# Kernel optimization log

Hardware: AMD Instinct MI355X
Metric: run time of the kernel (lower is better)

## Reference

```python
import jax, jax.numpy as jnp
import numpy as np

D_MODEL = 512
D_STATE = 16
D_CONV = 2
DT_RANK = D_MODEL // 16  # mamba default dt_rank = ceil(d_model/16)
D_INNER = D_MODEL        # expand = 1
B, L = 4, 2048
LN_EPS = 1e-5


def setup_inputs() -> dict:
    key = jax.random.key(0)
    ks = jax.random.split(key, 16)
    s = 0.02
    inp = {
        "x_signal": jax.random.normal(ks[0], (B, L, D_MODEL), jnp.float32),
        "x_stats": jax.random.normal(ks[1], (B, 1, D_MODEL), jnp.float32),
        # GatedCrossAttention params (torch Linear weight layout: (out, in))
        "gW1": jax.random.normal(ks[2], (D_MODEL, 2 * D_MODEL), jnp.float32) * s,
        "gb1": jnp.zeros((D_MODEL,), jnp.float32),
        "gW2": jax.random.normal(ks[3], (1, D_MODEL), jnp.float32) * s,
        "gb2": jnp.zeros((1,), jnp.float32),
        "ln_g": jnp.ones((D_MODEL,), jnp.float32),
        "ln_b": jnp.zeros((D_MODEL,), jnp.float32),
        # Mamba params
        "in_proj_W": jax.random.normal(ks[4], (2 * D_INNER, D_MODEL), jnp.float32) * s,
        "conv_w": jax.random.normal(ks[5], (D_INNER, D_CONV), jnp.float32) * s,
        "conv_b": jnp.zeros((D_INNER,), jnp.float32),
        "x_proj_W": jax.random.normal(ks[6], (DT_RANK + 2 * D_STATE, D_INNER), jnp.float32) * s,
        "dt_proj_W": jax.random.normal(ks[7], (D_INNER, DT_RANK), jnp.float32) * s,
        "dt_proj_b": jnp.full((D_INNER,), -4.6, jnp.float32),  # softplus ~ 0.01
        "A_log": jnp.log(jnp.broadcast_to(jnp.arange(1, D_STATE + 1, dtype=jnp.float32), (D_INNER, D_STATE))),
        "Dp": jnp.ones((D_INNER,), jnp.float32),
        "out_proj_W": jax.random.normal(ks[8], (D_MODEL, D_INNER), jnp.float32) * s,
    }
    return inp


def _silu(x):
    return x * jax.nn.sigmoid(x)


def _forward(x_signal, x_stats, gW1, gb1, gW2, gb2, ln_g, ln_b,
             in_proj_W, conv_w, conv_b, x_proj_W, dt_proj_W, dt_proj_b,
             A_log, Dp, out_proj_W):
    # ---- GatedCrossAttention ----
    xs = jnp.broadcast_to(x_stats, x_signal.shape)           # (B,L,D)
    gi = jnp.concatenate([x_signal, xs], axis=-1)            # (B,L,2D)
    h = jax.nn.relu(gi @ gW1.T + gb1)
    gate = jax.nn.sigmoid(h @ gW2.T + gb2)                   # (B,L,1)
    x = x_signal + gate * xs
    mu = jnp.mean(x, -1, keepdims=True)
    var = jnp.var(x, -1, keepdims=True)
    x = (x - mu) * jax.lax.rsqrt(var + LN_EPS) * ln_g + ln_b  # (B,L,D)

    # ---- Mamba (d_state=16, d_conv=2, expand=1) ----
    xz = x @ in_proj_W.T                                     # (B,L,2*Din)
    u, z = jnp.split(xz, 2, axis=-1)
    # causal depthwise conv1d, kernel size 2
    up = jnp.pad(u, ((0, 0), (D_CONV - 1, 0), (0, 0)))
    uc = conv_b + sum(conv_w[:, k] * up[:, k:k + u.shape[1]] for k in range(D_CONV))
    u = _silu(uc)                                            # (B,L,Din)

    xdbc = u @ x_proj_W.T                                    # (B,L,dt_rank+2N)
    dt = xdbc[..., :DT_RANK]
    Bm = xdbc[..., DT_RANK:DT_RANK + D_STATE]                # (B,L,N)
    Cm = xdbc[..., DT_RANK + D_STATE:]                       # (B,L,N)
    delta = jax.nn.softplus(dt @ dt_proj_W.T + dt_proj_b)    # (B,L,Din)

    A = -jnp.exp(A_log)                                      # (Din,N)
    dA = jnp.exp(delta[..., None] * A)                       # (B,L,Din,N)
    dBu = delta[..., None] * Bm[:, :, None, :] * u[..., None]

    def step(hst, inps):
        dA_t, dBu_t, C_t = inps
        hst = dA_t * hst + dBu_t                             # (B,Din,N)
        y_t = jnp.einsum('bdn,bn->bd', hst, C_t)
        return hst, y_t

    h0 = jnp.zeros((u.shape[0], D_INNER, D_STATE), u.dtype)
    xs_scan = (jnp.swapaxes(dA, 0, 1), jnp.swapaxes(dBu, 0, 1), jnp.swapaxes(Cm, 0, 1))
    _, ys = jax.lax.scan(step, h0, xs_scan)                  # (L,B,Din)
    y = jnp.swapaxes(ys, 0, 1) + Dp * u
    y = y * _silu(z)
    out = y @ out_proj_W.T                                   # (B,L,D)
    # dropout is identity in eval mode
    return out


def reference(x_signal, x_stats, gW1, gb1, gW2, gb2, ln_g, ln_b,
              in_proj_W, conv_w, conv_b, x_proj_W, dt_proj_W, dt_proj_b,
              A_log, Dp, out_proj_W):
    return _forward(x_signal, x_stats, gW1, gb1, gW2, gb2, ln_g, ln_b,
                    in_proj_W, conv_w, conv_b, x_proj_W, dt_proj_W, dt_proj_b,
                    A_log, Dp, out_proj_W)
```

## Files before the change

### kernel.cpp

```cpp
#include <hip/hip_runtime.h>
#include <hip/hip_bf16.h>
#include <math.h>

#define D_MODEL 512
#define D_STATE 16
#define DT_RANK 32
#define D_INNER 512
#define BB 4
#define LL 2048
#define MROWS (BB * LL)
#define LN_EPS 1e-5f
#define CHUNK 16
#define NCH (LL / CHUNK)
#define LOG2E 1.44269504f
#define LN2 0.69314718f

typedef __bf16 bf16x8 __attribute__((ext_vector_type(8)));
typedef float f32x4 __attribute__((ext_vector_type(4)));

__device__ __forceinline__ ushort f2bf(float x) {
  uint u = __float_as_uint(x);
  u = (u + 0x7fffu + ((u >> 16) & 1u)) >> 16;
  return (ushort)u;
}
__device__ __forceinline__ float bf2f(ushort h) {
  return __uint_as_float(((uint)h) << 16);
}
__device__ __forceinline__ void split2(float x, ushort& hi, ushort& lo) {
  hi = f2bf(x);
  lo = f2bf(x - bf2f(hi));
}

__device__ __forceinline__ void gload_lds16(const void* g, void* l) {
  __builtin_amdgcn_global_load_lds(
      (const __attribute__((address_space(1))) uint32_t*)g,
      (__attribute__((address_space(3))) uint32_t*)l, 16, 0, 0);
}

template <int EPI>
__global__ __launch_bounds__(256) void gemm_mfma(const ushort* __restrict__ Ahi,
                                                 const ushort* __restrict__ Alo,
                                                 const ushort* __restrict__ Bhi,
                                                 const ushort* __restrict__ Blo,
                                                 float* __restrict__ C, int ldc, int K,
                                                 int nx, const float* __restrict__ e0,
                                                 const float* __restrict__ g2,
                                                 float* __restrict__ sdot) {
  __shared__ ushort sA[2][2][128][32];
  __shared__ ushort sB[2][2][64][32];

  const int tid = threadIdx.x;
  const int lane = tid & 63;
  const int wid = tid >> 6;

  const int nwg = gridDim.x;
  const int q = nwg >> 3;
  const int t = (blockIdx.x & 7) * q + (blockIdx.x >> 3);
  const int bx = t % nx;
  const int by = t / nx;
  const int m0 = by * 128;
  const int n0 = bx * 64;

  const int srow = tid >> 2;
  const int koff = (((tid & 3) ^ ((tid >> 3) & 3)) << 3);
  const ushort* Ah_p = Ahi + (size_t)(m0 + srow) * K + koff;
  const ushort* Al_p = Alo + (size_t)(m0 + srow) * K + koff;
  const ushort* Bh_p = Bhi + (size_t)(n0 + srow) * K + koff;
  const ushort* Bl_p = Blo + (size_t)(n0 + srow) * K + koff;
  const size_t rstep = (size_t)64 * K;
  const int wb = wid * 16;

  const int wr = wid >> 1, wc = wid & 1;
  const int fr = lane & 15;
  const int rcs = (((lane >> 4) ^ ((fr >> 1) & 3)) << 3);

  f32x4 acc[4][2] = {};

  auto STAGE = [&](int bq, int kk) {
    gload_lds16(Ah_p + kk,         &sA[bq][0][wb][0]);
    gload_lds16(Ah_p + kk + rstep, &sA[bq][0][64 + wb][0]);
    gload_lds16(Al_p + kk,         &sA[bq][1][wb][0]);
    gload_lds16(Al_p + kk + rstep, &sA[bq][1][64 + wb][0]);
    gload_lds16(Bh_p + kk,         &sB[bq][0][wb][0]);
    gload_lds16(Bl_p + kk,         &sB[bq][1][wb][0]);
  };

  int cur = 0;
  STAGE(0, 0);
  __syncthreads();

  for (int k0 = 0; k0 < K; k0 += 32) {
    if (k0 + 32 < K) STAGE(cur ^ 1, k0 + 32);
    bf16x8 ah[4], al[4], bh[2], bl[2];
#pragma unroll
    for (int m = 0; m < 4; ++m) {
      const int ar = wr * 64 + m * 16 + fr;
      ah[m] = *(const bf16x8*)&sA[cur][0][ar][rcs];
      al[m] = *(const bf16x8*)&sA[cur][1][ar][rcs];
    }
#pragma unroll
    for (int n = 0; n < 2; ++n) {
      const int br = wc * 32 + n * 16 + fr;
      bh[n] = *(const bf16x8*)&sB[cur][0][br][rcs];
      bl[n] = *(const bf16x8*)&sB[cur][1][br][rcs];
    }
#pragma unroll
    for (int m = 0; m < 4; ++m)
#pragma unroll
      for (int n = 0; n < 2; ++n) {
        acc[m][n] = __builtin_amdgcn_mfma_f32_16x16x32_bf16(ah[m], bh[n],
                                                            acc[m][n], 0, 0, 0);
        acc[m][n] = __builtin_amdgcn_mfma_f32_16x16x32_bf16(ah[m], bl[n],
                                                            acc[m][n], 0, 0, 0);
        acc[m][n] = __builtin_amdgcn_mfma_f32_16x16x32_bf16(al[m], bh[n],
                                                            acc[m][n], 0, 0, 0);
      }
    __syncthreads();
    cur ^= 1;
  }

  const int rbase = (lane >> 4) * 4;
  if (EPI == 1) {
    const int c0 = n0 + wc * 32 + fr;
    const int c1c = n0 + wc * 32 + 16 + fr;
    const float g2a = g2[c0];
    const float g2b = g2[c1c];
#pragma unroll
    for (int m = 0; m < 4; ++m) {
#pragma unroll
      for (int r = 0; r < 4; ++r) {
        const int row = m0 + wr * 64 + m * 16 + rbase + r;
        const int bofs = (row >> 11) * D_MODEL;
        const float v0 = fmaxf(acc[m][0][r] + e0[bofs + c0], 0.f);
        const float v1 = fmaxf(acc[m][1][r] + e0[bofs + c1c], 0.f);
        float val = fmaf(v0, g2a, v1 * g2b);
        val += __shfl_xor(val, 1);
        val += __shfl_xor(val, 2);
        val += __shfl_xor(val, 4);
        val += __shfl_xor(val, 8);
        if (fr == 0) atomicAdd(&sdot[row], val);
      }
    }
  } else {
#pragma unroll
    for (int m = 0; m < 4; ++m) {
      const int row0 = m0 + wr * 64 + m * 16 + rbase;
#pragma unroll
      for (int n = 0; n < 2; ++n) {
        const int col = n0 + wc * 32 + n * 16 + fr;
#pragma unroll
        for (int r = 0; r < 4; ++r) {
          float v = acc[m][n][r];
          const int row = row0 + r;
          if (EPI == 2) {
            const float x = v + e0[col];
            const float e = __builtin_amdgcn_exp2f(-fabsf(x) * LOG2E);
            v = fmaxf(x, 0.f) + __log2f(1.f + e) * LN2;
          }
          C[(size_t)row * ldc + col] = v;
        }
      }
    }
  }
}

__global__ __launch_bounds__(256) void bc_gemm(const ushort* __restrict__ Ahi,
                                               const ushort* __restrict__ Alo,
                                               const ushort* __restrict__ Bhi,
                                               const ushort* __restrict__ Blo,
                                               float* __restrict__ BC) {
  __shared__ ushort sA[2][2][64][32];
  __shared__ ushort sB[2][2][32][32];
  const int K = 512;
  const int tid = threadIdx.x;
  const int lane = tid & 63;
  const int wid = tid >> 6;
  const int m0 = blockIdx.x * 64;

  const int srow = lane >> 2;
  const int koff = (((lane & 3) ^ ((lane >> 3) & 3)) << 3);
  const ushort* Ah_p = Ahi + (size_t)(m0 + wid * 16 + srow) * K + koff;
  const ushort* Al_p = Alo + (size_t)(m0 + wid * 16 + srow) * K + koff;
  const ushort* B_p = ((wid < 2) ? Bhi : Blo) + (size_t)((wid & 1) * 16 + srow) * K + koff;

  const int wr = wid >> 1, wc = wid & 1;
  const int fr = lane & 15;
  const int rcs = (((lane >> 4) ^ ((fr >> 1) & 3)) << 3);

  f32x4 acc[2] = {};

  auto STAGE = [&](int bq, int kk) {
    gload_lds16(Ah_p + kk, &sA[bq][0][wid * 16][0]);
    gload_lds16(Al_p + kk, &sA[bq][1][wid * 16][0]);
    gload_lds16(B_p + kk, &sB[bq][wid >> 1][(wid & 1) * 16][0]);
  };

  int cur = 0;
  STAGE(0, 0);
  __syncthreads();

  for (int k0 = 0; k0 < K; k0 += 32) {
    if (k0 + 32 < K) STAGE(cur ^ 1, k0 + 32);
    bf16x8 ah[2], al[2], bh, bl;
#pragma unroll
    for (int m = 0; m < 2; ++m) {
      const int ar = wr * 32 + m * 16 + fr;
      ah[m] = *(const bf16x8*)&sA[cur][0][ar][rcs];
      al[m] = *(const bf16x8*)&sA[cur][1][ar][rcs];
    }
    const int br = wc * 16 + fr;
    bh = *(const bf16x8*)&sB[cur][0][br][rcs];
    bl = *(const bf16x8*)&sB[cur][1][br][rcs];
#pragma unroll
    for (int m = 0; m < 2; ++m) {
      acc[m] = __builtin_amdgcn_mfma_f32_16x16x32_bf16(ah[m], bh, acc[m], 0, 0, 0);
      acc[m] = __builtin_amdgcn_mfma_f32_16x16x32_bf16(ah[m], bl, acc[m], 0, 0, 0);
      acc[m] = __builtin_amdgcn_mfma_f32_16x16x32_bf16(al[m], bh, acc[m], 0, 0, 0);
    }
    __syncthreads();
    cur ^= 1;
  }

  const int rbase = (lane >> 4) * 4;
  const int col = wc * 16 + fr;
#pragma unroll
  for (int m = 0; m < 2; ++m) {
    const int row0 = m0 + wr * 32 + m * 16 + rbase;
#pragma unroll
    for (int r = 0; r < 4; ++r)
      BC[(size_t)(row0 + r) * 32 + col] = acc[m][r];
  }
}

__global__ __launch_bounds__(256) void split_x(const float* __restrict__ x,
                                               ushort* __restrict__ hi,
                                               ushort* __restrict__ lo) {
  const int i = (blockIdx.x * 256 + threadIdx.x) * 4;
  float4 v = *(const float4*)(x + i);
  ushort h0, l0, h1, l1, h2, l2, h3, l3;
  split2(v.x, h0, l0); split2(v.y, h1, l1); split2(v.z, h2, l2); split2(v.w, h3, l3);
  ushort4 hv = {h0, h1, h2, h3}, lv = {l0, l1, l2, l3};
  *(ushort4*)(hi + i) = hv;
  *(ushort4*)(lo + i) = lv;
}

__global__ __launch_bounds__(128) void prep_w(const float* __restrict__ gW1,
                                              const float* __restrict__ ipW,
                                              const float* __restrict__ opW,
                                              const float* __restrict__ xW,
                                              const float* __restrict__ dtW,
                                              ushort* __restrict__ Whi,
                                              ushort* __restrict__ Wlo) {
  const int r = blockIdx.x;
  const int t = threadIdx.x;
  float v[4];
  if (r < 2048) {
    const float* src;
    if (r < 512) src = gW1 + (size_t)r * 1024;
    else if (r < 1536) src = ipW + (size_t)(r - 512) * 512;
    else src = opW + (size_t)(r - 1536) * 512;
    const float4 xv = *(const float4*)(src + t * 4);
    v[0] = xv.x; v[1] = xv.y; v[2] = xv.z; v[3] = xv.w;
  } else {
    const int j = r - 2048;
    v[0] = v[1] = v[2] = v[3] = 0.f;
    if (j < 512) {
      __shared__ float sdt[32];
      if (t < 32) sdt[t] = dtW[j * 32 + t];
      __syncthreads();
      const int k = t * 4;
#pragma unroll 8
      for (int rr = 0; rr < 32; ++rr) {
        const float w = sdt[rr];
        const float4 xv = *(const float4*)(xW + rr * 512 + k);
        v[0] = fmaf(w, xv.x, v[0]);
        v[1] = fmaf(w, xv.y, v[1]);
        v[2] = fmaf(w, xv.z, v[2]);
        v[3] = fmaf(w, xv.w, v[3]);
      }
    } else {
      const float4 xv = *(const float4*)(xW + (size_t)(32 + j - 512) * 512 + t * 4);
      v[0] = xv.x; v[1] = xv.y; v[2] = xv.z; v[3] = xv.w;
    }
  }
  ushort h[4], l[4];
#pragma unroll
  for (int c = 0; c < 4; ++c) split2(v[c], h[c], l[c]);
  const size_t off = (size_t)r * 512 + t * 4;
  ushort4 hv = {h[0], h[1], h[2], h[3]}, lv = {l[0], l[1], l[2], l[3]};
  *(ushort4*)(Whi + off) = hv;
  *(ushort4*)(Wlo + off) = lv;
}

__global__ __launch_bounds__(512) void c1_kernel(const float* __restrict__ xstats,
                                                 const float* __restrict__ gW1,
                                                 const float* __restrict__ gb1,
                                                 float* __restrict__ c1) {
  const int b = blockIdx.x;
  const int j = threadIdx.x;
  float acc = gb1[j];
  const float* xs = xstats + b * D_MODEL;
  const float* w = gW1 + (size_t)j * (2 * D_MODEL) + D_MODEL;
  for (int k = 0; k < D_MODEL; k += 4) {
    acc = fmaf(xs[k], w[k], acc);
    acc = fmaf(xs[k + 1], w[k + 1], acc);
    acc = fmaf(xs[k + 2], w[k + 2], acc);
    acc = fmaf(xs[k + 3], w[k + 3], acc);
  }
  c1[b * D_MODEL + j] = acc;
}

__device__ __forceinline__ float block_sum(float v, float* sm) {
#pragma unroll
  for (int m = 32; m; m >>= 1) v += __shfl_xor(v, m);
  const int lane = threadIdx.x & 63, w = threadIdx.x >> 6;
  __syncthreads();
  if (!lane) sm[w] = v;
  __syncthreads();
  return sm[0] + sm[1] + sm[2] + sm[3];
}

__global__ __launch_bounds__(256) void gate_ln_kernel(const float* __restrict__ sdot,
                                                      const float* __restrict__ xsig,
                                                      const float* __restrict__ xstats,
                                                      const float* __restrict__ gb2,
                                                      const float* __restrict__ ln_g,
                                                      const float* __restrict__ ln_b,
                                                      ushort* __restrict__ XNhi,
                                                      ushort* __restrict__ XNlo) {
  __shared__ float red[4];
  const int row = blockIdx.x;
  const int b = row >> 11;
  const int tid = threadIdx.x;
  const size_t rb = (size_t)row * D_MODEL;

  const float gate = 1.f / (1.f + expf(-(sdot[row] + gb2[0])));

  float xr[2];
#pragma unroll
  for (int ii = 0; ii < 2; ++ii) {
    const int j = tid + ii * 256;
    xr[ii] = xsig[rb + j] + gate * xstats[b * D_MODEL + j];
  }
  float sv = xr[0] + xr[1];
  const float mu = block_sum(sv, red) * (1.f / D_MODEL);
  float s2 = (xr[0] - mu) * (xr[0] - mu) + (xr[1] - mu) * (xr[1] - mu);
  const float var = block_sum(s2, red) * (1.f / D_MODEL);
  const float inv = rsqrtf(var + LN_EPS);
#pragma unroll
  for (int ii = 0; ii < 2; ++ii) {
    const int j = tid + ii * 256;
    const float v = (xr[ii] - mu) * inv * ln_g[j] + ln_b[j];
    ushort h, l;
    split2(v, h, l);
    XNhi[rb + j] = h;
    XNlo[rb + j] = l;
  }
}

__global__ __launch_bounds__(256) void conv_silu_kernel(const float* __restrict__ XZ,
                                                        const float* __restrict__ conv_w,
                                                        const float* __restrict__ conv_b,
                                                        ushort* __restrict__ Uhi,
                                                        ushort* __restrict__ Ulo) {
  const int row = blockIdx.x;
  const bool first = (row & (LL - 1)) == 0;
  const int tid = threadIdx.x;
#pragma unroll
  for (int ii = 0; ii < 2; ++ii) {
    const int j = tid + ii * 256;
    const float up = first ? 0.f : XZ[(size_t)(row - 1) * (2 * D_INNER) + j];
    const float uc = XZ[(size_t)row * (2 * D_INNER) + j];
    float v = conv_b[j] + conv_w[j * 2 + 0] * up + conv_w[j * 2 + 1] * uc;
    v = v / (1.f + expf(-v));
    ushort h, l;
    split2(v, h, l);
    Uhi[(size_t)row * D_INNER + j] = h;
    Ulo[(size_t)row * D_INNER + j] = l;
  }
}

__global__ __launch_bounds__(256) void scan_part1(const float* __restrict__ DELTA,
                                                  const ushort* __restrict__ Uhi,
                                                  const ushort* __restrict__ Ulo,
                                                  const float* __restrict__ BC,
                                                  const float* __restrict__ A_log,
                                                  float* __restrict__ SLOC,
                                                  float* __restrict__ DSUM) {
  __shared__ __align__(16) float sBC[CHUNK][32];
  const int tid = threadIdx.x;
  const int bid = blockIdx.x;
  const int d = ((bid & 1) << 8) + tid;
  const int c = (bid >> 1) & (NCH - 1);
  const int b = bid >> 8;
  const size_t base = (size_t)b * LL + (size_t)c * CHUNK;

  {
    const int row = tid >> 4, col = (tid & 15) << 1;
    *(float2*)&sBC[row][col] = *(const float2*)(BC + (base + row) * 32 + col);
  }
  float A2[16];
#pragma unroll
  for (int n = 0; n < 16; ++n) A2[n] = -expf(A_log[d * 16 + n]) * LOG2E;
  __syncthreads();

  float S[16];
#pragma unroll
  for (int n = 0; n < 16; ++n) S[n] = 0.f;
  float dsum = 0.f;

#pragma unroll 2
  for (int t = 0; t < CHUNK; ++t) {
    const size_t r = base + t;
    const float delta = DELTA[r * D_INNER + d];
    const float u = bf2f(Uhi[r * D_INNER + d]) + bf2f(Ulo[r * D_INNER + d]);
    dsum += delta;
    const float du = delta * u;
    float Bv[16];
#pragma unroll
    for (int i = 0; i < 4; ++i)
      *(float4*)&Bv[i * 4] = *(const float4*)&sBC[t][i * 4];
#pragma unroll
    for (int n = 0; n < 16; ++n) {
      const float dA = __builtin_amdgcn_exp2f(delta * A2[n]);
      S[n] = fmaf(dA, S[n], du * Bv[n]);
    }
  }
  const size_t ci = ((size_t)b * NCH + c) * D_INNER + d;
#pragma unroll
  for (int i = 0; i < 4; ++i)
    *(float4*)(SLOC + ci * 16 + i * 4) = *(const float4*)&S[i * 4];
  DSUM[ci] = dsum;
}

__global__ __launch_bounds__(256) void scan_combine(const float* __restrict__ SLOC,
                                                    const float* __restrict__ DSUM,
                                                    const float* __restrict__ A_log,
                                                    float* __restrict__ HINIT) {
  const int idx = blockIdx.x * 256 + threadIdx.x;
  const int b = idx >> 13;
  const int d = (idx >> 4) & (D_INNER - 1);
  const int n = idx & 15;
  const float A2 = -expf(A_log[d * D_STATE + n]) * LOG2E;
  float h = 0.f;
#pragma unroll 4
  for (int c = 0; c < NCH; ++c) {
    const size_t ci = ((size_t)b * NCH + c) * D_INNER + d;
    HINIT[ci * 16 + n] = h;
    const float a = __builtin_amdgcn_exp2f(A2 * DSUM[ci]);
    h = fmaf(a, h, SLOC[ci * 16 + n]);
  }
}

__global__ __launch_bounds__(256) void scan_part3(const float* __restrict__ DELTA,
                                                  const ushort* __restrict__ Uhi,
                                                  const ushort* __restrict__ Ulo,
                                                  const float* __restrict__ BC,
                                                  const float* __restrict__ XZ,
                                                  const float* __restrict__ A_log,
                                                  const float* __restrict__ Dp,
                                                  const float* __restrict__ HINIT,
                                                  ushort* __restrict__ Yhi,
                                                  ushort* __restrict__ Ylo) {
  __shared__ __align__(16) float sBC[CHUNK][32];
  const int tid = threadIdx.x;
  const int bid = blockIdx.x;
  const int d = ((bid & 1) << 8) + tid;
  const int c = (bid >> 1) & (NCH - 1);
  const int b = bid >> 8;
  const size_t base = (size_t)b * LL + (size_t)c * CHUNK;

  {
    const int row = tid >> 4, col = (tid & 15) << 1;
    *(float2*)&sBC[row][col] = *(const float2*)(BC + (base + row) * 32 + col);
  }
  float A2[16];
#pragma unroll
  for (int n = 0; n < 16; ++n) A2[n] = -expf(A_log[d * 16 + n]) * LOG2E;
  const float Dpd = Dp[d];

  const size_t ci = ((size_t)b * NCH + c) * D_INNER + d;
  float h[16];
#pragma unroll
  for (int i = 0; i < 4; ++i)
    *(float4*)&h[i * 4] = *(const float4*)(HINIT + ci * 16 + i * 4);
  __syncthreads();

#pragma unroll 2
  for (int t = 0; t < CHUNK; ++t) {
    const size_t r = base + t;
    const float delta = DELTA[r * D_INNER + d];
    const float u = bf2f(Uhi[r * D_INNER + d]) + bf2f(Ulo[r * D_INNER + d]);
    const float z = XZ[r * (2 * D_INNER) + D_INNER + d];
    const float du = delta * u;
    float BCv[32];
#pragma unroll
    for (int i = 0; i < 8; ++i)
      *(float4*)&BCv[i * 4] = *(const float4*)&sBC[t][i * 4];
    float y = 0.f;
#pragma unroll
    for (int n = 0; n < 16; ++n) {
      const float dA = __builtin_amdgcn_exp2f(delta * A2[n]);
      h[n] = fmaf(dA, h[n], du * BCv[n]);
      y = fmaf(h[n], BCv[16 + n], y);
    }
    const float sz = z / (1.f + __builtin_amdgcn_exp2f(-z * LOG2E));
    const float o = (y + Dpd * u) * sz;
    ushort hh, ll;
    split2(o, hh, ll);
    Yhi[r * D_INNER + d] = hh;
    Ylo[r * D_INNER + d] = ll;
  }
}

extern "C" void kernel_launch(void* const* d_in, const int* in_sizes, int n_in,
                              void* d_out, int out_size, void* d_ws, size_t ws_size,
                              hipStream_t stream) {
  const float* x_signal = (const float*)d_in[0];
  const float* x_stats  = (const float*)d_in[1];
  const float* gW1      = (const float*)d_in[2];
  const float* gb1      = (const float*)d_in[3];
  const float* gW2      = (const float*)d_in[4];
  const float* gb2      = (const float*)d_in[5];
  const float* ln_g     = (const float*)d_in[6];
  const float* ln_b     = (const float*)d_in[7];
  const float* in_proj_W = (const float*)d_in[8];
  const float* conv_w   = (const float*)d_in[9];
  const float* conv_b   = (const float*)d_in[10];
  const float* x_proj_W = (const float*)d_in[11];
  const float* dt_proj_W = (const float*)d_in[12];
  const float* dt_proj_b = (const float*)d_in[13];
  const float* A_log    = (const float*)d_in[14];
  const float* Dp       = (const float*)d_in[15];
  const float* out_proj_W = (const float*)d_in[16];
  float* out = (float*)d_out;

  float* ws = (float*)d_ws;
  const size_t NE = (size_t)MROWS * D_MODEL;
  float* H    = ws;
  float* XNf  = H + NE;
  float* XZ   = XNf + NE;
  float* UHL  = XZ + 2 * NE;
  float* BC   = UHL + NE;
  float* C1   = BC + (size_t)MROWS * 32;
  float* SGATE = C1 + BB * D_MODEL;
  float* SLOC = SGATE + MROWS;
  float* DSUM = SLOC + (size_t)BB * NCH * D_INNER * D_STATE;
  float* HINIT = DSUM + (size_t)BB * NCH * D_INNER;
  float* WSP  = HINIT + (size_t)BB * NCH * D_INNER * D_STATE;

  ushort* XNhi = (ushort*)XNf;
  ushort* XNlo = XNhi + NE;
  ushort* XShi = (ushort*)XZ;
  ushort* XSlo = XShi + NE;
  ushort* Yhi  = (ushort*)H;
  ushort* Ylo  = Yhi + NE;
  ushort* Uhi  = (ushort*)UHL;
  ushort* Ulo  = Uhi + NE;
  ushort* Whi  = (ushort*)WSP;
  ushort* Wlo  = Whi + (size_t)2592 * 512;
  float* DELTA = XNf;

  hipMemsetAsync(SGATE, 0, MROWS * sizeof(float), stream);
  split_x<<<dim3(NE / 1024), dim3(256), 0, stream>>>(x_signal, XShi, XSlo);
  prep_w<<<dim3(2592), dim3(128), 0, stream>>>(gW1, in_proj_W, out_proj_W, x_proj_W,
                                               dt_proj_W, Whi, Wlo);

  c1_kernel<<<dim3(BB), dim3(512), 0, stream>>>(x_stats, gW1, gb1, C1);

  gemm_mfma<1><<<dim3(8 * 64), dim3(256), 0, stream>>>(
      XShi, XSlo, Whi, Wlo, nullptr, 0, D_MODEL, 8, C1, gW2, SGATE);

  gate_ln_kernel<<<dim3(MROWS), dim3(256), 0, stream>>>(SGATE, x_signal, x_stats,
                                                        gb2, ln_g, ln_b, XNhi, XNlo);

  gemm_mfma<0><<<dim3(16 * 64), dim3(256), 0, stream>>>(
      XNhi, XNlo, Whi + (size_t)512 * 512, Wlo + (size_t)512 * 512, XZ, 2 * D_INNER,
      D_MODEL, 16, nullptr, nullptr, nullptr);

  conv_silu_kernel<<<dim3(MROWS), dim3(256), 0, stream>>>(XZ, conv_w, conv_b, Uhi, Ulo);

  gemm_mfma<2><<<dim3(8 * 64), dim3(256), 0, stream>>>(
      Uhi, Ulo, Whi + (size_t)2048 * 512, Wlo + (size_t)2048 * 512, DELTA, 512,
      D_MODEL, 8, dt_proj_b, nullptr, nullptr);

  bc_gemm<<<dim3(MROWS / 64), dim3(256), 0, stream>>>(
      Uhi, Ulo, Whi + (size_t)2560 * 512, Wlo + (size_t)2560 * 512, BC);

  scan_part1<<<dim3(BB * NCH * 2), dim3(256), 0, stream>>>(DELTA, Uhi, Ulo, BC, A_log,
                                                           SLOC, DSUM);
  scan_combine<<<dim3(128), dim3(256), 0, stream>>>(SLOC, DSUM, A_log, HINIT);
  scan_part3<<<dim3(BB * NCH * 2), dim3(256), 0, stream>>>(DELTA, Uhi, Ulo, BC, XZ,
                                                           A_log, Dp, HINIT, Yhi, Ylo);

  gemm_mfma<0><<<dim3(8 * 64), dim3(256), 0, stream>>>(
      Yhi, Ylo, Whi + (size_t)1536 * 512, Wlo + (size_t)1536 * 512, out, D_MODEL,
      D_INNER, 8, nullptr, nullptr, nullptr);
}
```

Measured before the change: 219.9 us.

## Load GEMM B-operands directly to registers, fuse prep kernels, double scan chunk

The MFMA GEMMs stop staging the weight (B) tiles through LDS and instead prefetch them from global memory straight into registers, double-buffered alongside the A staging. bc_gemm is retiled to 32-row blocks with one A tile per wave. split_x, prep_w and c1 are merged into a single prep_all launch, and conv_silu now processes 16 rows per block with paired-channel vector accesses and a fast exp2. The scan chunk size goes from 16 to 32, halving the chunk count. Together these aim to cut LDS traffic, barrier work and launch overhead, but the per-wave global B loads may be less coalesced and longer chunks lengthen the serial scan per thread.

```diff
diff --git a/kernel.cpp b/kernel.cpp
--- a/kernel.cpp
+++ b/kernel.cpp
@@ -10,7 +10,7 @@
 #define LL 2048
 #define MROWS (BB * LL)
 #define LN_EPS 1e-5f
-#define CHUNK 16
+#define CHUNK 32
 #define NCH (LL / CHUNK)
 #define LOG2E 1.44269504f
 #define LN2 0.69314718f
@@ -47,7 +47,6 @@
                                                  const float* __restrict__ g2,
                                                  float* __restrict__ sdot) {
   __shared__ ushort sA[2][2][128][32];
-  __shared__ ushort sB[2][2][64][32];
 
   const int tid = threadIdx.x;
   const int lane = tid & 63;
@@ -65,14 +64,19 @@
   const int koff = (((tid & 3) ^ ((tid >> 3) & 3)) << 3);
   const ushort* Ah_p = Ahi + (size_t)(m0 + srow) * K + koff;
   const ushort* Al_p = Alo + (size_t)(m0 + srow) * K + koff;
-  const ushort* Bh_p = Bhi + (size_t)(n0 + srow) * K + koff;
-  const ushort* Bl_p = Blo + (size_t)(n0 + srow) * K + koff;
   const size_t rstep = (size_t)64 * K;
   const int wb = wid * 16;
 
   const int wr = wid >> 1, wc = wid & 1;
   const int fr = lane & 15;
+  const int fk = (lane >> 4) * 8;
   const int rcs = (((lane >> 4) ^ ((fr >> 1) & 3)) << 3);
+
+  const size_t boff = (size_t)(n0 + wc * 32 + fr) * K + fk;
+  const ushort* Bh0 = Bhi + boff;
+  const ushort* Bl0 = Blo + boff;
+  const ushort* Bh1 = Bh0 + (size_t)16 * K;
+  const ushort* Bl1 = Bl0 + (size_t)16 * K;
 
   f32x4 acc[4][2] = {};
 
@@ -81,17 +85,26 @@
     gload_lds16(Ah_p + kk + rstep, &sA[bq][0][64 + wb][0]);
     gload_lds16(Al_p + kk,         &sA[bq][1][wb][0]);
     gload_lds16(Al_p + kk + rstep, &sA[bq][1][64 + wb][0]);
-    gload_lds16(Bh_p + kk,         &sB[bq][0][wb][0]);
-    gload_lds16(Bl_p + kk,         &sB[bq][1][wb][0]);
   };
 
+  bf16x8 bhc[2], blc[2];
+  bhc[0] = *(const bf16x8*)Bh0;  bhc[1] = *(const bf16x8*)Bh1;
+  blc[0] = *(const bf16x8*)Bl0;  blc[1] = *(const bf16x8*)Bl1;
   int cur = 0;
   STAGE(0, 0);
   __syncthreads();
 
   for (int k0 = 0; k0 < K; k0 += 32) {
-    if (k0 + 32 < K) STAGE(cur ^ 1, k0 + 32);
-    bf16x8 ah[4], al[4], bh[2], bl[2];
+    bf16x8 bhn[2], bln[2];
+    const bool more = (k0 + 32 < K);
+    if (more) {
+      STAGE(cur ^ 1, k0 + 32);
+      bhn[0] = *(const bf16x8*)(Bh0 + k0 + 32);
+      bhn[1] = *(const bf16x8*)(Bh1 + k0 + 32);
+      bln[0] = *(const bf16x8*)(Bl0 + k0 + 32);
+      bln[1] = *(const bf16x8*)(Bl1 + k0 + 32);
+    }
+    bf16x8 ah[4], al[4];
 #pragma unroll
     for (int m = 0; m < 4; ++m) {
       const int ar = wr * 64 + m * 16 + fr;
@@ -99,24 +112,22 @@
       al[m] = *(const bf16x8*)&sA[cur][1][ar][rcs];
     }
 #pragma unroll
-    for (int n = 0; n < 2; ++n) {
-      const int br = wc * 32 + n * 16 + fr;
-      bh[n] = *(const bf16x8*)&sB[cur][0][br][rcs];
-      bl[n] = *(const bf16x8*)&sB[cur][1][br][rcs];
-    }
-#pragma unroll
     for (int m = 0; m < 4; ++m)
 #pragma unroll
       for (int n = 0; n < 2; ++n) {
-        acc[m][n] = __builtin_amdgcn_mfma_f32_16x16x32_bf16(ah[m], bh[n],
+        acc[m][n] = __builtin_amdgcn_mfma_f32_16x16x32_bf16(ah[m], bhc[n],
                                                             acc[m][n], 0, 0, 0);
-        acc[m][n] = __builtin_amdgcn_mfma_f32_16x16x32_bf16(ah[m], bl[n],
+        acc[m][n] = __builtin_amdgcn_mfma_f32_16x16x32_bf16(ah[m], blc[n],
                                                             acc[m][n], 0, 0, 0);
-        acc[m][n] = __builtin_amdgcn_mfma_f32_16x16x32_bf16(al[m], bh[n],
+        acc[m][n] = __builtin_amdgcn_mfma_f32_16x16x32_bf16(al[m], bhc[n],
                                                             acc[m][n], 0, 0, 0);
       }
     __syncthreads();
     cur ^= 1;
+    if (more) {
+      bhc[0] = bhn[0]; bhc[1] = bhn[1];
+      blc[0] = bln[0]; blc[1] = bln[1];
+    }
   }
 
   const int rbase = (lane >> 4) * 4;
@@ -169,109 +180,111 @@
                                                const ushort* __restrict__ Bhi,
                                                const ushort* __restrict__ Blo,
                                                float* __restrict__ BC) {
-  __shared__ ushort sA[2][2][64][32];
-  __shared__ ushort sB[2][2][32][32];
+  __shared__ ushort sA[2][2][32][32];
   const int K = 512;
   const int tid = threadIdx.x;
   const int lane = tid & 63;
   const int wid = tid >> 6;
-  const int m0 = blockIdx.x * 64;
+  const int m0 = blockIdx.x * 32;
 
   const int srow = lane >> 2;
   const int koff = (((lane & 3) ^ ((lane >> 3) & 3)) << 3);
-  const ushort* Ah_p = Ahi + (size_t)(m0 + wid * 16 + srow) * K + koff;
-  const ushort* Al_p = Alo + (size_t)(m0 + wid * 16 + srow) * K + koff;
-  const ushort* B_p = ((wid < 2) ? Bhi : Blo) + (size_t)((wid & 1) * 16 + srow) * K + koff;
+  const ushort* A_p = ((wid < 2) ? Ahi : Alo) +
+                      (size_t)(m0 + (wid & 1) * 16 + srow) * K + koff;
 
   const int wr = wid >> 1, wc = wid & 1;
   const int fr = lane & 15;
+  const int fk = (lane >> 4) * 8;
   const int rcs = (((lane >> 4) ^ ((fr >> 1) & 3)) << 3);
-
-  f32x4 acc[2] = {};
+  const size_t boff = (size_t)(wc * 16 + fr) * K + fk;
+  const ushort* Bh = Bhi + boff;
+  const ushort* Bl = Blo + boff;
+
+  f32x4 acc = {};
 
   auto STAGE = [&](int bq, int kk) {
-    gload_lds16(Ah_p + kk, &sA[bq][0][wid * 16][0]);
-    gload_lds16(Al_p + kk, &sA[bq][1][wid * 16][0]);
-    gload_lds16(B_p + kk, &sB[bq][wid >> 1][(wid & 1) * 16][0]);
+    gload_lds16(A_p + kk, &sA[bq][wid >> 1][(wid & 1) * 16][0]);
   };
 
+  bf16x8 bhc = *(const bf16x8*)Bh;
+  bf16x8 blc = *(const bf16x8*)Bl;
   int cur = 0;
   STAGE(0, 0);
   __syncthreads();
 
   for (int k0 = 0; k0 < K; k0 += 32) {
-    if (k0 + 32 < K) STAGE(cur ^ 1, k0 + 32);
-    bf16x8 ah[2], al[2], bh, bl;
-#pragma unroll
-    for (int m = 0; m < 2; ++m) {
-      const int ar = wr * 32 + m * 16 + fr;
-      ah[m] = *(const bf16x8*)&sA[cur][0][ar][rcs];
-      al[m] = *(const bf16x8*)&sA[cur][1][ar][rcs];
-    }
-    const int br = wc * 16 + fr;
-    bh = *(const bf16x8*)&sB[cur][0][br][rcs];
-    bl = *(const bf16x8*)&sB[cur][1][br][rcs];
-#pragma unroll
-    for (int m = 0; m < 2; ++m) {
-      acc[m] = __builtin_amdgcn_mfma_f32_16x16x32_bf16(ah[m], bh, acc[m], 0, 0, 0);
-      acc[m] = __builtin_amdgcn_mfma_f32_16x16x32_bf16(ah[m], bl, acc[m], 0, 0, 0);
-      acc[m] = __builtin_amdgcn_mfma_f32_16x16x32_bf16(al[m], bh, acc[m], 0, 0, 0);
-    }
+    bf16x8 bhn, bln;
+    const bool more = (k0 + 32 < K);
+    if (more) {
+      STAGE(cur ^ 1, k0 + 32);
+      bhn = *(const bf16x8*)(Bh + k0 + 32);
+      bln = *(const bf16x8*)(Bl + k0 + 32);
+    }
+    const int ar = wr * 16 + fr;
+    bf16x8 ah = *(const bf16x8*)&sA[cur][0][ar][rcs];
+    bf16x8 al = *(const bf16x8*)&sA[cur][1][ar][rcs];
+    acc = __builtin_amdgcn_mfma_f32_16x16x32_bf16(ah, bhc, acc, 0, 0, 0);
+    acc = __builtin_amdgcn_mfma_f32_16x16x32_bf16(ah, blc, acc, 0, 0, 0);
+    acc = __builtin_amdgcn_mfma_f32_16x16x32_bf16(al, bhc, acc, 0, 0, 0);
     __syncthreads();
     cur ^= 1;
+    if (more) { bhc = bhn; blc = bln; }
   }
 
   const int rbase = (lane >> 4) * 4;
   const int col = wc * 16 + fr;
-#pragma unroll
-  for (int m = 0; m < 2; ++m) {
-    const int row0 = m0 + wr * 32 + m * 16 + rbase;
-#pragma unroll
-    for (int r = 0; r < 4; ++r)
-      BC[(size_t)(row0 + r) * 32 + col] = acc[m][r];
-  }
-}
-
-__global__ __launch_bounds__(256) void split_x(const float* __restrict__ x,
-                                               ushort* __restrict__ hi,
-                                               ushort* __restrict__ lo) {
-  const int i = (blockIdx.x * 256 + threadIdx.x) * 4;
-  float4 v = *(const float4*)(x + i);
-  ushort h0, l0, h1, l1, h2, l2, h3, l3;
-  split2(v.x, h0, l0); split2(v.y, h1, l1); split2(v.z, h2, l2); split2(v.w, h3, l3);
-  ushort4 hv = {h0, h1, h2, h3}, lv = {l0, l1, l2, l3};
-  *(ushort4*)(hi + i) = hv;
-  *(ushort4*)(lo + i) = lv;
-}
-
-__global__ __launch_bounds__(128) void prep_w(const float* __restrict__ gW1,
-                                              const float* __restrict__ ipW,
-                                              const float* __restrict__ opW,
-                                              const float* __restrict__ xW,
-                                              const float* __restrict__ dtW,
-                                              ushort* __restrict__ Whi,
-                                              ushort* __restrict__ Wlo) {
-  const int r = blockIdx.x;
-  const int t = threadIdx.x;
-  float v[4];
-  if (r < 2048) {
-    const float* src;
-    if (r < 512) src = gW1 + (size_t)r * 1024;
-    else if (r < 1536) src = ipW + (size_t)(r - 512) * 512;
-    else src = opW + (size_t)(r - 1536) * 512;
-    const float4 xv = *(const float4*)(src + t * 4);
-    v[0] = xv.x; v[1] = xv.y; v[2] = xv.z; v[3] = xv.w;
-  } else {
+  const int row0 = m0 + wr * 16 + rbase;
+#pragma unroll
+  for (int r = 0; r < 4; ++r)
+    BC[(size_t)(row0 + r) * 32 + col] = acc[r];
+}
+
+__global__ __launch_bounds__(256) void prep_all(const float* __restrict__ x,
+                                                const float* __restrict__ gW1,
+                                                const float* __restrict__ ipW,
+                                                const float* __restrict__ opW,
+                                                const float* __restrict__ xW,
+                                                const float* __restrict__ dtW,
+                                                const float* __restrict__ xstats,
+                                                const float* __restrict__ gb1,
+                                                ushort* __restrict__ XShi,
+                                                ushort* __restrict__ XSlo,
+                                                ushort* __restrict__ Whi,
+                                                ushort* __restrict__ Wlo,
+                                                float* __restrict__ c1) {
+  const int blk = blockIdx.x;
+  const int tid = threadIdx.x;
+  if (blk < 4096) {
+    const int i = (blk * 256 + tid) * 4;
+    float4 v = *(const float4*)(x + i);
+    ushort h0, l0, h1, l1, h2, l2, h3, l3;
+    split2(v.x, h0, l0); split2(v.y, h1, l1);
+    split2(v.z, h2, l2); split2(v.w, h3, l3);
+    ushort4 hv = {h0, h1, h2, h3}, lv = {l0, l1, l2, l3};
+    *(ushort4*)(XShi + i) = hv;
+    *(ushort4*)(XSlo + i) = lv;
+    return;
+  }
+  if (blk < 4096 + 1296) {
+    const int sub = tid >> 7;
+    const int tt = tid & 127;
+    const int r = (blk - 4096) * 2 + sub;
     const int j = r - 2048;
-    v[0] = v[1] = v[2] = v[3] = 0.f;
-    if (j < 512) {
-      __shared__ float sdt[32];
-      if (t < 32) sdt[t] = dtW[j * 32 + t];
-      __syncthreads();
-      const int k = t * 4;
+    __shared__ float sdt[2][32];
+    if (tt < 32 && j >= 0 && j < 512) sdt[sub][tt] = dtW[j * 32 + tt];
+    __syncthreads();
+    float v[4] = {0.f, 0.f, 0.f, 0.f};
+    if (r < 2048) {
+      const float* src = (r < 512)    ? gW1 + (size_t)r * 1024
+                         : (r < 1536) ? ipW + (size_t)(r - 512) * 512
+                                      : opW + (size_t)(r - 1536) * 512;
+      const float4 xv = *(const float4*)(src + tt * 4);
+      v[0] = xv.x; v[1] = xv.y; v[2] = xv.z; v[3] = xv.w;
+    } else if (j < 512) {
+      const int k = tt * 4;
 #pragma unroll 8
       for (int rr = 0; rr < 32; ++rr) {
-        const float w = sdt[rr];
+        const float w = sdt[sub][rr];
         const float4 xv = *(const float4*)(xW + rr * 512 + k);
         v[0] = fmaf(w, xv.x, v[0]);
         v[1] = fmaf(w, xv.y, v[1]);
@@ -279,25 +292,21 @@
         v[3] = fmaf(w, xv.w, v[3]);
       }
     } else {
-      const float4 xv = *(const float4*)(xW + (size_t)(32 + j - 512) * 512 + t * 4);
+      const float4 xv = *(const float4*)(xW + (size_t)(32 + j - 512) * 512 + tt * 4);
       v[0] = xv.x; v[1] = xv.y; v[2] = xv.z; v[3] = xv.w;
     }
-  }
-  ushort h[4], l[4];
-#pragma unroll
-  for (int c = 0; c < 4; ++c) split2(v[c], h[c], l[c]);
-  const size_t off = (size_t)r * 512 + t * 4;
-  ushort4 hv = {h[0], h[1], h[2], h[3]}, lv = {l[0], l[1], l[2], l[3]};
-  *(ushort4*)(Whi + off) = hv;
-  *(ushort4*)(Wlo + off) = lv;
-}
-
-__global__ __launch_bounds__(512) void c1_kernel(const float* __restrict__ xstats,
-                                                 const float* __restrict__ gW1,
-                                                 const float* __restrict__ gb1,
-                                                 float* __restrict__ c1) {
-  const int b = blockIdx.x;
-  const int j = threadIdx.x;
+    ushort h[4], l[4];
+#pragma unroll
+    for (int c = 0; c < 4; ++c) split2(v[c], h[c], l[c]);
+    const size_t off = (size_t)r * 512 + tt * 4;
+    ushort4 hv = {h[0], h[1], h[2], h[3]}, lv = {l[0], l[1], l[2], l[3]};
+    *(ushort4*)(Whi + off) = hv;
+    *(ushort4*)(Wlo + off) = lv;
+    return;
+  }
+  const int c = blk - (4096 + 1296);
+  const int b = c >> 1;
+  const int j = ((c & 1) << 8) + tid;
   float acc = gb1[j];
   const float* xs = xstats + b * D_MODEL;
   const float* w = gW1 + (size_t)j * (2 * D_MODEL) + D_MODEL;
@@ -363,20 +372,32 @@
                                                         const float* __restrict__ conv_b,
                                                         ushort* __restrict__ Uhi,
                                                         ushort* __restrict__ Ulo) {
-  const int row = blockIdx.x;
-  const bool first = (row & (LL - 1)) == 0;
-  const int tid = threadIdx.x;
-#pragma unroll
-  for (int ii = 0; ii < 2; ++ii) {
-    const int j = tid + ii * 256;
-    const float up = first ? 0.f : XZ[(size_t)(row - 1) * (2 * D_INNER) + j];
-    const float uc = XZ[(size_t)row * (2 * D_INNER) + j];
-    float v = conv_b[j] + conv_w[j * 2 + 0] * up + conv_w[j * 2 + 1] * uc;
-    v = v / (1.f + expf(-v));
-    ushort h, l;
-    split2(v, h, l);
-    Uhi[(size_t)row * D_INNER + j] = h;
-    Ulo[(size_t)row * D_INNER + j] = l;
+  const int base = blockIdx.x * 16;
+  const int j = threadIdx.x * 2;
+  const float w0a = conv_w[j * 2 + 0], w1a = conv_w[j * 2 + 1];
+  const float w0b = conv_w[j * 2 + 2], w1b = conv_w[j * 2 + 3];
+  const float ba = conv_b[j], bb = conv_b[j + 1];
+  float2 prev;
+  if ((base & (LL - 1)) == 0) {
+    prev.x = 0.f; prev.y = 0.f;
+  } else {
+    prev = *(const float2*)(XZ + (size_t)(base - 1) * (2 * D_INNER) + j);
+  }
+#pragma unroll 4
+  for (int t = 0; t < 16; ++t) {
+    const size_t r = base + t;
+    const float2 cur = *(const float2*)(XZ + r * (2 * D_INNER) + j);
+    float va = ba + w0a * prev.x + w1a * cur.x;
+    float vb = bb + w0b * prev.y + w1b * cur.y;
+    va = va / (1.f + __builtin_amdgcn_exp2f(-va * LOG2E));
+    vb = vb / (1.f + __builtin_amdgcn_exp2f(-vb * LOG2E));
+    ushort ha, la, hb, lb;
+    split2(va, ha, la);
+    split2(vb, hb, lb);
+    ushort2 hv = {ha, hb}, lv = {la, lb};
+    *(ushort2*)(Uhi + r * D_INNER + j) = hv;
+    *(ushort2*)(Ulo + r * D_INNER + j) = lv;
+    prev = cur;
   }
 }
 
@@ -392,12 +413,12 @@
   const int bid = blockIdx.x;
   const int d = ((bid & 1) << 8) + tid;
   const int c = (bid >> 1) & (NCH - 1);
-  const int b = bid >> 8;
+  const int b = bid >> 7;
   const size_t base = (size_t)b * LL + (size_t)c * CHUNK;
 
   {
-    const int row = tid >> 4, col = (tid & 15) << 1;
-    *(float2*)&sBC[row][col] = *(const float2*)(BC + (base + row) * 32 + col);
+    const int row = tid >> 3, col = (tid & 7) << 2;
+    *(float4*)&sBC[row][col] = *(const float4*)(BC + (base + row) * 32 + col);
   }
   float A2[16];
 #pragma unroll
@@ -467,12 +488,12 @@
   const int bid = blockIdx.x;
   const int d = ((bid & 1) << 8) + tid;
   const int c = (bid >> 1) & (NCH - 1);
-  const int b = bid >> 8;
+  const int b = bid >> 7;
   const size_t base = (size_t)b * LL + (size_t)c * CHUNK;
 
   {
-    const int row = tid >> 4, col = (tid & 15) << 1;
-    *(float2*)&sBC[row][col] = *(const float2*)(BC + (base + row) * 32 + col);
+    const int row = tid >> 3, col = (tid & 7) << 2;
+    *(float4*)&sBC[row][col] = *(const float4*)(BC + (base + row) * 32 + col);
   }
   float A2[16];
 #pragma unroll
@@ -562,11 +583,9 @@
   float* DELTA = XNf;
 
   hipMemsetAsync(SGATE, 0, MROWS * sizeof(float), stream);
-  split_x<<<dim3(NE / 1024), dim3(256), 0, stream>>>(x_signal, XShi, XSlo);
-  prep_w<<<dim3(2592), dim3(128), 0, stream>>>(gW1, in_proj_W, out_proj_W, x_proj_W,
-                                               dt_proj_W, Whi, Wlo);
-
-  c1_kernel<<<dim3(BB), dim3(512), 0, stream>>>(x_stats, gW1, gb1, C1);
+  prep_all<<<dim3(4096 + 1296 + 8), dim3(256), 0, stream>>>(
+      x_signal, gW1, in_proj_W, out_proj_W, x_proj_W, dt_proj_W, x_stats, gb1,
+      XShi, XSlo, Whi, Wlo, C1);
 
   gemm_mfma<1><<<dim3(8 * 64), dim3(256), 0, stream>>>(
       XShi, XSlo, Whi, Wlo, nullptr, 0, D_MODEL, 8, C1, gW2, SGATE);
@@ -578,13 +597,14 @@
       XNhi, XNlo, Whi + (size_t)512 * 512, Wlo + (size_t)512 * 512, XZ, 2 * D_INNER,
       D_MODEL, 16, nullptr, nullptr, nullptr);
 
-  conv_silu_kernel<<<dim3(MROWS), dim3(256), 0, stream>>>(XZ, conv_w, conv_b, Uhi, Ulo);
+  conv_silu_kernel<<<dim3(MROWS / 16), dim3(256), 0, stream>>>(XZ, conv_w, conv_b,
+                                                               Uhi, Ulo);
 
   gemm_mfma<2><<<dim3(8 * 64), dim3(256), 0, stream>>>(
       Uhi, Ulo, Whi + (size_t)2048 * 512, Wlo + (size_t)2048 * 512, DELTA, 512,
       D_MODEL, 8, dt_proj_b, nullptr, nullptr);
 
-  bc_gemm<<<dim3(MROWS / 64), dim3(256), 0, stream>>>(
+  bc_gemm<<<dim3(MROWS / 32), dim3(256), 0, stream>>>(
       Uhi, Ulo, Whi + (size_t)2560 * 512, Wlo + (size_t)2560 * 512, BC);
 
   scan_part1<<<dim3(BB * NCH * 2), dim3(256), 0, stream>>>(DELTA, Uhi, Ulo, BC, A_log,
```

Result: slower. 230.7 us (+4.9%).
